# Performance work log

Measured on AMD Instinct MI355X. Metric: run time of the kernel, lower is better.

Reference implementation:

```python
import jax, jax.numpy as jnp
import numpy as np

N_PAPER, N_AUTHOR, E = 100000, 50000, 1000000
D_PAPER, D_AUTHOR, HID, OUT = 256, 128, 256, 349


def setup_inputs() -> dict:
    key = jax.random.key(0)
    ks = jax.random.split(key, 16)
    s = 0.05
    return {
        'x_paper': jax.random.normal(ks[0], (N_PAPER, D_PAPER), jnp.float32),
        'x_author': jax.random.normal(ks[1], (N_AUTHOR, D_AUTHOR), jnp.float32),
        'cites': jax.random.randint(ks[2], (2, E), 0, N_PAPER, jnp.int64 if jax.config.jax_enable_x64 else jnp.int32),
        'writes_src': jax.random.randint(ks[3], (E,), 0, N_AUTHOR),
        'writes_dst': jax.random.randint(ks[4], (E,), 0, N_PAPER),
        'gcn_W1': jax.random.normal(ks[5], (D_PAPER, HID), jnp.float32) * s,
        'gcn_b1': jnp.zeros((HID,), jnp.float32),
        'sage_Wl1': jax.random.normal(ks[6], (D_AUTHOR, HID), jnp.float32) * s,
        'sage_bl1': jnp.zeros((HID,), jnp.float32),
        'sage_Wr1': jax.random.normal(ks[7], (D_PAPER, HID), jnp.float32) * s,
        'gcn_W2': jax.random.normal(ks[8], (HID, HID), jnp.float32) * s,
        'gcn_b2': jnp.zeros((HID,), jnp.float32),
        'sage_Wl2': jax.random.normal(ks[9], (D_AUTHOR, HID), jnp.float32) * s,
        'sage_bl2': jnp.zeros((HID,), jnp.float32),
        'sage_Wr2': jax.random.normal(ks[10], (HID, HID), jnp.float32) * s,
        'lin_W': jax.random.normal(ks[11], (HID, OUT), jnp.float32) * s,
        'lin_b': jnp.zeros((OUT,), jnp.float32),
    }


def _gcn_conv(x, W, b, src, dst, n):
    # GCNConv with add_self_loops=True, symmetric normalization
    loop = jnp.arange(n, dtype=src.dtype)
    si = jnp.concatenate([src, loop])
    di = jnp.concatenate([dst, loop])
    deg = jax.ops.segment_sum(jnp.ones_like(di, x.dtype), di, n)
    dinv = jnp.where(deg > 0, jax.lax.rsqrt(jnp.maximum(deg, 1.0)), 0.0)
    norm = dinv[si] * dinv[di]  # [E+n]
    h = x @ W                   # [n, hid]
    out = jax.ops.segment_sum(h[si] * norm[:, None], di, n)
    return out + b


def _sage_conv(x_src, x_dst, Wl, bl, Wr, src, dst, n_dst):
    # SAGEConv: mean-aggregate neighbors -> lin_l, plus root lin_r (no bias)
    agg = jax.ops.segment_sum(x_src[src], dst, n_dst)
    cnt = jax.ops.segment_sum(jnp.ones_like(dst, x_src.dtype), dst, n_dst)
    mean = agg / jnp.maximum(cnt, 1.0)[:, None]
    return mean @ Wl + bl + x_dst @ Wr


def reference(x_paper, x_author, cites, writes_src, writes_dst,
              gcn_W1, gcn_b1, sage_Wl1, sage_bl1, sage_Wr1,
              gcn_W2, gcn_b2, sage_Wl2, sage_bl2, sage_Wr2,
              lin_W, lin_b):
    n = x_paper.shape[0]
    c_src, c_dst = cites[0], cites[1]
    # layer 1: HeteroConv with aggr='sum' over the two edge-type outputs
    p = jax.nn.relu(
        _gcn_conv(x_paper, gcn_W1, gcn_b1, c_src, c_dst, n)
        + _sage_conv(x_author, x_paper, sage_Wl1, sage_bl1, sage_Wr1, writes_src, writes_dst, n))
    # layer 2 (author features are never updated by these edge types)
    p = jax.nn.relu(
        _gcn_conv(p, gcn_W2, gcn_b2, c_src, c_dst, n)
        + _sage_conv(x_author, p, sage_Wl2, sage_bl2, sage_Wr2, writes_src, writes_dst, n))
    return p @ lin_W + lin_b
```

## Files before the change

kernel.cpp:

```cpp
#include <hip/hip_runtime.h>


#define DP   256
#define DA   128
#define HIDN 256
#define DOUT 349
#define NBKT 782
#define CHUNK 4096

typedef unsigned short u16;
typedef unsigned int u32;
typedef __attribute__((ext_vector_type(8))) short bf16x8;
typedef __attribute__((ext_vector_type(4))) float f32x4;

__device__ __forceinline__ u16 bf16_rn(float x) {
  union { float f; unsigned u; } v; v.f = x;
  unsigned r = v.u + 0x7FFFu + ((v.u >> 16) & 1u);
  return (u16)(r >> 16);
}
__device__ __forceinline__ float bf16f(u16 h) {
  union { float f; unsigned u; } v; v.u = ((unsigned)h) << 16; return v.f;
}
__device__ __forceinline__ unsigned pack2(float a, float b) {
  return (unsigned)bf16_rn(a) | ((unsigned)bf16_rn(b) << 16);
}

__device__ __forceinline__ void gload16(const void* g, void* lds) {
  __builtin_amdgcn_global_load_lds(
      (const __attribute__((address_space(1))) unsigned int*)g,
      (__attribute__((address_space(3))) unsigned int*)lds, 16, 0, 0);
}

#define SCAN_TPB 256
#define SCAN_VPT 8
#define SCAN_TILE 2048

__global__ void scan_local(const int* __restrict__ in, int* __restrict__ out,
                           int* __restrict__ bsum, int n) {
  __shared__ int sdata[SCAN_TPB];
  int t = threadIdx.x;
  int base = blockIdx.x * SCAN_TILE + t * SCAN_VPT;
  int v[SCAN_VPT];
  int sum = 0;
#pragma unroll
  for (int j = 0; j < SCAN_VPT; ++j) {
    int idx = base + j;
    v[j] = (idx < n) ? in[idx] : 0;
    sum += v[j];
  }
  sdata[t] = sum;
  __syncthreads();
  for (int off = 1; off < SCAN_TPB; off <<= 1) {
    int x = (t >= off) ? sdata[t - off] : 0;
    __syncthreads();
    sdata[t] += x;
    __syncthreads();
  }
  int prefix = sdata[t] - sum;
  if (t == SCAN_TPB - 1) bsum[blockIdx.x] = sdata[t];
  int run = prefix;
#pragma unroll
  for (int j = 0; j < SCAN_VPT; ++j) {
    int idx = base + j;
    if (idx < n) out[idx] = run;
    run += v[j];
  }
}

__global__ void scan_spine(int* __restrict__ bsum, int nb) {
  __shared__ int sdata[256];
  int t = threadIdx.x;
  int v = (t < nb) ? bsum[t] : 0;
  sdata[t] = v;
  __syncthreads();
  for (int off = 1; off < 256; off <<= 1) {
    int x = (t >= off) ? sdata[t - off] : 0;
    __syncthreads();
    sdata[t] += x;
    __syncthreads();
  }
  if (t < nb) bsum[t] = sdata[t] - v;
}

__global__ void scan_add(int* __restrict__ out, const int* __restrict__ bsum, int n) {
  int add = bsum[blockIdx.x];
  int base = blockIdx.x * SCAN_TILE + threadIdx.x * SCAN_VPT;
#pragma unroll
  for (int j = 0; j < SCAN_VPT; ++j) {
    int idx = base + j;
    if (idx < n) out[idx] += add;
  }
}

__global__ __launch_bounds__(256) void sort_pass1(
    const int* __restrict__ src, const int* __restrict__ dst,
    uint2* __restrict__ tmp, int* __restrict__ gcount, int* __restrict__ lofs,
    int E, int nch) {
  const int c = blockIdx.x, t = threadIdx.x;
  __shared__ u32 cnt[NBKT];
  __shared__ u32 ofs[NBKT];
  __shared__ u32 sdata[256];
  __shared__ uint2 stage[CHUNK];

  for (int i = t; i < NBKT; i += 256) cnt[i] = 0;
  __syncthreads();
  const int base = c * CHUNK;
#pragma unroll
  for (int j = 0; j < 16; ++j) {
    int i = t + j * 256, idx = base + i;
    if (idx < E) {
      uint2 e; e.x = (u32)src[idx]; e.y = (u32)dst[idx];
      stage[i] = e;
      atomicAdd(&cnt[e.y >> 7], 1u);
    }
  }
  __syncthreads();
  for (int i = t; i < NBKT; i += 256) gcount[(size_t)i * nch + c] = (int)cnt[i];
  u32 ssum = 0;
  const int b0 = t * 4;
#pragma unroll
  for (int j = 0; j < 4; ++j) {
    int i = b0 + j;
    if (i < NBKT) ssum += cnt[i];
  }
  sdata[t] = ssum;
  __syncthreads();
  for (int o = 1; o < 256; o <<= 1) {
    u32 x = (t >= o) ? sdata[t - o] : 0;
    __syncthreads();
    sdata[t] += x;
    __syncthreads();
  }
  u32 run = sdata[t] - ssum;
#pragma unroll
  for (int j = 0; j < 4; ++j) {
    int i = b0 + j;
    if (i < NBKT) { ofs[i] = run; run += cnt[i]; }
  }
  __syncthreads();
  for (int i = t; i < NBKT; i += 256) {
    lofs[(size_t)c * NBKT + i] = (int)ofs[i];
    cnt[i] = ofs[i];
  }
  __syncthreads();
#pragma unroll
  for (int j = 0; j < 16; ++j) {
    int i = t + j * 256, idx = base + i;
    if (idx < E) {
      uint2 e = stage[i];
      u32 p = atomicAdd(&cnt[e.y >> 7], 1u);
      tmp[(size_t)base + p] = e;
    }
  }
}

#define MAXB 2560
__global__ __launch_bounds__(256) void sort_pass2(
    const uint2* __restrict__ tmp, const int* __restrict__ prefix,
    const int* __restrict__ gcount, const int* __restrict__ lofs,
    int* __restrict__ outSorted, int* __restrict__ deg, int* __restrict__ offArr,
    int E, int nch, int n) {
  const int b = blockIdx.x, t = threadIdx.x;
  __shared__ u32 est[MAXB];
  __shared__ u32 outl[MAXB];
  __shared__ u32 cnt[128], ofs[128];
  __shared__ u32 sdata[256];

  const int node0 = b << 7;
  const int ebase = prefix[(size_t)b * nch];
  const int eend = (b == (int)gridDim.x - 1) ? E : prefix[(size_t)(b + 1) * nch];
  const int esize = eend - ebase;

  for (int c = t; c < nch; c += 256) {
    int g = lofs[(size_t)c * NBKT + b];
    int len = gcount[(size_t)b * nch + c];
    int dp = prefix[(size_t)b * nch + c] - ebase;
    for (int k = 0; k < len; ++k) {
      uint2 e = tmp[(size_t)c * CHUNK + g + k];
      est[dp + k] = (e.x << 7) | (e.y & 127u);
    }
  }
  if (t < 128) cnt[t] = 0;
  __syncthreads();
  for (int i = t; i < esize; i += 256) atomicAdd(&cnt[est[i] & 127u], 1u);
  __syncthreads();
  u32 v = (t < 128) ? cnt[t] : 0;
  sdata[t] = v;
  __syncthreads();
  for (int o = 1; o < 256; o <<= 1) {
    u32 x = (t >= o) ? sdata[t - o] : 0;
    __syncthreads();
    sdata[t] += x;
    __syncthreads();
  }
  if (t < 128) ofs[t] = sdata[t] - v;
  __syncthreads();
  const int nNodes = (n - node0) < 128 ? (n - node0) : 128;
  if (t < nNodes) {
    deg[node0 + t] = (int)cnt[t];
    offArr[node0 + t] = ebase + (int)ofs[t];
  }
  __syncthreads();
  if (t < 128) cnt[t] = ofs[t];
  __syncthreads();
  for (int i = t; i < esize; i += 256) {
    u32 e = est[i];
    u32 p = atomicAdd(&cnt[e & 127u], 1u);
    outl[p] = e >> 7;
  }
  __syncthreads();
  for (int i = t; i < esize; i += 256) outSorted[ebase + i] = (int)outl[i];
}

__global__ void conv_bf16(const float* __restrict__ x, u16* __restrict__ o, int n8) {
  int i = blockIdx.x * blockDim.x + threadIdx.x;
  if (i >= n8) return;
  const float4* x4 = (const float4*)x;
  float4 v0 = x4[(size_t)i * 2];
  float4 v1 = x4[(size_t)i * 2 + 1];
  uint4 O;
  O.x = pack2(v0.x, v0.y);
  O.y = pack2(v0.z, v0.w);
  O.z = pack2(v1.x, v1.y);
  O.w = pack2(v1.z, v1.w);
  ((uint4*)o)[i] = O;
}

__global__ void prep_weight(const float* __restrict__ W, int K, int N, int Npad,
                            u16* __restrict__ Bt) {
  int idx = blockIdx.x * blockDim.x + threadIdx.x;
  int tot = Npad * K;
  if (idx >= tot) return;
  int n = idx / K, k = idx - n * K;
  float v = (n < N) ? W[(size_t)k * N + n] : 0.f;
  Bt[idx] = bf16_rn(v);
}

__global__ void pad_bias(const float* __restrict__ a, const float* __restrict__ b,
                         float* __restrict__ o, int n, int npad) {
  int i = blockIdx.x * blockDim.x + threadIdx.x;
  if (i < npad) o[i] = (i < n) ? (a[i] + (b ? b[i] : 0.f)) : 0.f;
}

__global__ void node_prep(const u16* __restrict__ xa16,
                          const int* __restrict__ w_off, const int* __restrict__ w_cnt,
                          const int* __restrict__ w_sorted,
                          const int* __restrict__ deg_c,
                          u16* __restrict__ mean, float* __restrict__ dinv, int n) {
  int wave = (blockIdx.x * blockDim.x + threadIdx.x) >> 6;
  int lane = threadIdx.x & 63;
  if (wave >= n) return;
  int d = wave;
  int start = w_off[d];
  int cnt = w_cnt[d];
  float ax = 0.f, ay = 0.f;
  const unsigned* xa = (const unsigned*)xa16;
  for (int j0 = 0; j0 < cnt; j0 += 64) {
    int nn = cnt - j0; nn = nn < 64 ? nn : 64;
    int sl = (j0 + lane < cnt) ? w_sorted[start + j0 + lane] : 0;
    int jj = 0;
    for (; jj + 4 <= nn; jj += 4) {
      int s0 = __shfl(sl, jj), s1 = __shfl(sl, jj + 1);
      int s2 = __shfl(sl, jj + 2), s3 = __shfl(sl, jj + 3);
      unsigned v0 = xa[(size_t)s0 * 64 + lane];
      unsigned v1 = xa[(size_t)s1 * 64 + lane];
      unsigned v2 = xa[(size_t)s2 * 64 + lane];
      unsigned v3 = xa[(size_t)s3 * 64 + lane];
      ax += bf16f((u16)v0) + bf16f((u16)v1) + bf16f((u16)v2) + bf16f((u16)v3);
      ay += bf16f((u16)(v0 >> 16)) + bf16f((u16)(v1 >> 16)) +
            bf16f((u16)(v2 >> 16)) + bf16f((u16)(v3 >> 16));
    }
    for (; jj < nn; ++jj) {
      int s = __shfl(sl, jj);
      unsigned v = xa[(size_t)s * 64 + lane];
      ax += bf16f((u16)v);
      ay += bf16f((u16)(v >> 16));
    }
  }
  float inv = 1.0f / (float)((cnt > 0) ? cnt : 1);
  ((unsigned*)mean)[(size_t)d * 64 + lane] = pack2(ax * inv, ay * inv);
  if (lane == 0) dinv[d] = rsqrtf((float)(deg_c[d] + 1));
}

__global__ void agg_gcn(const u16* __restrict__ xin, const float* __restrict__ dinv,
                        const int* __restrict__ c_off, const int* __restrict__ c_cnt,
                        const int* __restrict__ c_sorted,
                        u16* __restrict__ xout, int n) {
  int wave = (blockIdx.x * blockDim.x + threadIdx.x) >> 6;
  int lane = threadIdx.x & 63;
  if (wave >= n) return;
  int d = wave;
  int start = c_off[d], cnt = c_cnt[d];
  float a0 = 0.f, a1 = 0.f, a2 = 0.f, a3 = 0.f;
  const uint2* base = (const uint2*)xin;
  for (int j0 = 0; j0 < cnt; j0 += 64) {
    int nn = cnt - j0; nn = nn < 64 ? nn : 64;
    int sl = (j0 + lane < cnt) ? c_sorted[start + j0 + lane] : 0;
    int jj = 0;
    for (; jj + 4 <= nn; jj += 4) {
      int s0 = __shfl(sl, jj), s1 = __shfl(sl, jj + 1);
      int s2 = __shfl(sl, jj + 2), s3 = __shfl(sl, jj + 3);
      float d0 = dinv[s0], d1 = dinv[s1], d2 = dinv[s2], d3 = dinv[s3];
      uint2 v0 = base[(size_t)s0 * 64 + lane];
      uint2 v1 = base[(size_t)s1 * 64 + lane];
      uint2 v2 = base[(size_t)s2 * 64 + lane];
      uint2 v3 = base[(size_t)s3 * 64 + lane];
      a0 = fmaf(bf16f((u16)v0.x), d0, a0); a1 = fmaf(bf16f((u16)(v0.x >> 16)), d0, a1);
      a2 = fmaf(bf16f((u16)v0.y), d0, a2); a3 = fmaf(bf16f((u16)(v0.y >> 16)), d0, a3);
      a0 = fmaf(bf16f((u16)v1.x), d1, a0); a1 = fmaf(bf16f((u16)(v1.x >> 16)), d1, a1);
      a2 = fmaf(bf16f((u16)v1.y), d1, a2); a3 = fmaf(bf16f((u16)(v1.y >> 16)), d1, a3);
      a0 = fmaf(bf16f((u16)v2.x), d2, a0); a1 = fmaf(bf16f((u16)(v2.x >> 16)), d2, a1);
      a2 = fmaf(bf16f((u16)v2.y), d2, a2); a3 = fmaf(bf16f((u16)(v2.y >> 16)), d2, a3);
      a0 = fmaf(bf16f((u16)v3.x), d3, a0); a1 = fmaf(bf16f((u16)(v3.x >> 16)), d3, a1);
      a2 = fmaf(bf16f((u16)v3.y), d3, a2); a3 = fmaf(bf16f((u16)(v3.y >> 16)), d3, a3);
    }
    for (; jj < nn; ++jj) {
      int s = __shfl(sl, jj);
      float ds = dinv[s];
      uint2 v = base[(size_t)s * 64 + lane];
      a0 = fmaf(bf16f((u16)v.x), ds, a0); a1 = fmaf(bf16f((u16)(v.x >> 16)), ds, a1);
      a2 = fmaf(bf16f((u16)v.y), ds, a2); a3 = fmaf(bf16f((u16)(v.y >> 16)), ds, a3);
    }
  }
  float dd = dinv[d];
  {
    uint2 v = base[(size_t)d * 64 + lane];
    a0 = fmaf(bf16f((u16)v.x), dd, a0); a1 = fmaf(bf16f((u16)(v.x >> 16)), dd, a1);
    a2 = fmaf(bf16f((u16)v.y), dd, a2); a3 = fmaf(bf16f((u16)(v.y >> 16)), dd, a3);
  }
  uint2 O;
  O.x = pack2(a0 * dd, a1 * dd);
  O.y = pack2(a2 * dd, a3 * dd);
  ((uint2*)xout)[(size_t)d * 64 + lane] = O;
}

template <int NSEG, bool F32OUT, int NC>
__global__ __launch_bounds__(512, 4) void gemm_bf16(
    const u16* __restrict__ A0, const u16* __restrict__ A1, const u16* __restrict__ A2,
    const u16* __restrict__ B0, const u16* __restrict__ B1, const u16* __restrict__ B2,
    const float* __restrict__ bias,
    u16* __restrict__ Cp, float* __restrict__ Cf,
    int M, int N) {
  __shared__ u16 Ah[2][4096];
  __shared__ u16 Bh[2][8192];

  const int t = threadIdx.x;
  const int wid = t >> 6, lane = t & 63;
  const int wr = wid >> 2, wc = wid & 3;
  const int lrow = lane & 15, kslot = lane >> 4;
  const int jsw = kslot ^ ((lrow >> 1) & 3);

  const int nb = gridDim.x;
  const int q = nb >> 3, r = nb & 7;
  const int xcd = blockIdx.x & 7, pos = blockIdx.x >> 3;
  const int lin = (xcd < r ? xcd * (q + 1) : r * (q + 1) + (xcd - r) * q) + pos;
  const int bx = lin / NC, by = lin - bx * NC;
  const int gm = bx * 128;
  const int gn = by * 256;

  const int s_r = lane >> 2;
  const int s_j = (lane & 3) ^ ((s_r >> 1) & 3);

  f32x4 acc[4][4];
  const f32x4 z4 = {0.f, 0.f, 0.f, 0.f};
#pragma unroll
  for (int m = 0; m < 4; ++m)
#pragma unroll
    for (int n = 0; n < 4; ++n) acc[m][n] = z4;

  const int NT = (NSEG == 3) ? 20 : 8;

  auto STAGE = [&](int tt, int half) {
    const u16* A;
    const u16* B;
    int rs, k0;
    if (NSEG == 3 && tt >= 16)     { A = A2; B = B2; rs = 128; k0 = (tt - 16) * 32; }
    else if (NSEG == 3 && tt >= 8) { A = A1; B = B1; rs = 256; k0 = (tt - 8) * 32; }
    else                           { A = A0; B = B0; rs = 256; k0 = tt * 32; }
    {
      int grow = gm + wid * 16 + s_r;
      grow = grow < M ? grow : M - 1;
      gload16(A + (size_t)grow * rs + (k0 + s_j * 8), &Ah[half][wid * 512]);
    }
#pragma unroll
    for (int c = 0; c < 2; ++c) {
      int chunk = wid * 2 + c;
      int col = gn + chunk * 16 + s_r;
      gload16(B + (size_t)col * rs + (k0 + s_j * 8), &Bh[half][chunk * 512]);
    }
  };

  STAGE(0, 0);
  __syncthreads();

  for (int tt = 0; tt < NT; ++tt) {
    const int half = tt & 1;
    if (tt + 1 < NT) STAGE(tt + 1, half ^ 1);

    bf16x8 ah[4];
    const int ab = (wr * 64 + lrow) * 32 + jsw * 8;
#pragma unroll
    for (int m = 0; m < 4; ++m) ah[m] = *(const bf16x8*)&Ah[half][ab + m * 512];
    const int bb = (wc * 64 + lrow) * 32 + jsw * 8;
#pragma unroll
    for (int n = 0; n < 4; ++n) {
      bf16x8 bn = *(const bf16x8*)&Bh[half][bb + n * 512];
#pragma unroll
      for (int m = 0; m < 4; ++m)
        acc[m][n] = __builtin_amdgcn_mfma_f32_16x16x32_bf16(ah[m], bn, acc[m][n], 0, 0, 0);
    }
    __syncthreads();
  }

  const int col0 = gn + wc * 64 + lrow;
  const int row00 = gm + wr * 64 + kslot * 4;
#pragma unroll
  for (int m = 0; m < 4; ++m) {
#pragma unroll
    for (int i = 0; i < 4; ++i) {
      int row = row00 + m * 16 + i;
      if (row >= M) continue;
#pragma unroll
      for (int n = 0; n < 4; ++n) {
        int col = col0 + n * 16;
        float v = acc[m][n][i] + bias[col];
        if (F32OUT) {
          if (col < N) Cf[(size_t)row * N + col] = v;
        } else {
          Cp[(size_t)row * 256 + col] = bf16_rn(fmaxf(v, 0.f));
        }
      }
    }
  }
}

static inline size_t align_up(size_t x) { return (x + 255) & ~(size_t)255; }

extern "C" void kernel_launch(void* const* d_in, const int* in_sizes, int n_in,
                              void* d_out, int out_size, void* d_ws, size_t ws_size,
                              hipStream_t stream) {
  const float* x_paper  = (const float*)d_in[0];
  const float* x_author = (const float*)d_in[1];
  const int*   cites    = (const int*)d_in[2];
  const int*   w_src    = (const int*)d_in[3];
  const int*   w_dst    = (const int*)d_in[4];
  const float* W1  = (const float*)d_in[5];
  const float* b1  = (const float*)d_in[6];
  const float* Wl1 = (const float*)d_in[7];
  const float* bl1 = (const float*)d_in[8];
  const float* Wr1 = (const float*)d_in[9];
  const float* W2  = (const float*)d_in[10];
  const float* b2  = (const float*)d_in[11];
  const float* Wl2 = (const float*)d_in[12];
  const float* bl2 = (const float*)d_in[13];
  const float* Wr2 = (const float*)d_in[14];
  const float* linW = (const float*)d_in[15];
  const float* linb = (const float*)d_in[16];
  float* out = (float*)d_out;

  const int N = in_sizes[0] / DP;
  const int NA = in_sizes[1] / DA;
  const int E = in_sizes[3];
  const int* c_src = cites;
  const int* c_dst = cites + E;

  const int NCH = (E + CHUNK - 1) / CHUNK;
  const int NB = (N + 127) >> 7;
  const int GC = NB * NCH;

  char* w = (char*)d_ws;
  size_t off = 0;
  auto alloc = [&](size_t bytes) -> void* {
    void* p = w + off;
    off = align_up(off + bytes);
    return p;
  };
  int* deg_c      = (int*)alloc((size_t)N * 4);
  int* cnt_w      = (int*)alloc((size_t)N * 4);
  int* cites_off  = (int*)alloc((size_t)N * 4);
  int* writes_off = (int*)alloc((size_t)N * 4);
  int* c_sorted   = (int*)alloc((size_t)E * 4);
  int* w_sorted   = (int*)alloc((size_t)E * 4);
  uint2* tmpE     = (uint2*)alloc((size_t)NCH * CHUNK * 8);
  int* gcount     = (int*)alloc((size_t)GC * 4);
  int* gprefix    = (int*)alloc((size_t)GC * 4);
  int* lofs       = (int*)alloc((size_t)NCH * NBKT * 4);
  int* bsumA      = (int*)alloc(256 * 4);
  float* dinv     = (float*)alloc((size_t)N * 4);
  u16* xa16       = (u16*)alloc((size_t)NA * DA * 2);
  u16* meanA      = (u16*)alloc((size_t)N * DA * 2);
  u16* xp         = (u16*)alloc((size_t)N * 256 * 2);
  u16* xs         = (u16*)alloc((size_t)N * 256 * 2);
  u16* pb         = (u16*)alloc((size_t)N * 256 * 2);
  const int bsW = 256 * 256, bsL = 256 * 128, bsLin = 512 * 256;
  u16* BtW1  = (u16*)alloc((size_t)bsW * 2);
  u16* BtWr1 = (u16*)alloc((size_t)bsW * 2);
  u16* BtW2  = (u16*)alloc((size_t)bsW * 2);
  u16* BtWr2 = (u16*)alloc((size_t)bsW * 2);
  u16* BtWl1 = (u16*)alloc((size_t)bsL * 2);
  u16* BtWl2 = (u16*)alloc((size_t)bsL * 2);
  u16* BtLin = (u16*)alloc((size_t)bsLin * 2);
  float* biasR1  = (float*)alloc(256 * 4);
  float* biasR2  = (float*)alloc(256 * 4);
  float* biasLin = (float*)alloc(512 * 4);
  (void)ws_size; (void)n_in; (void)out_size;

  const int nsb2 = (GC + SCAN_TILE - 1) / SCAN_TILE;

  sort_pass1<<<NCH, 256, 0, stream>>>(c_src, c_dst, tmpE, gcount, lofs, E, NCH);
  scan_local<<<nsb2, SCAN_TPB, 0, stream>>>(gcount, gprefix, bsumA, GC);
  scan_spine<<<1, 256, 0, stream>>>(bsumA, nsb2);
  scan_add<<<nsb2, SCAN_TPB, 0, stream>>>(gprefix, bsumA, GC);
  sort_pass2<<<NB, 256, 0, stream>>>(tmpE, gprefix, gcount, lofs,
                                     c_sorted, deg_c, cites_off, E, NCH, N);

  conv_bf16<<<(N * 32 + 255) / 256, 256, 0, stream>>>(x_paper, xp, N * 32);
  conv_bf16<<<(NA * 16 + 255) / 256, 256, 0, stream>>>(x_author, xa16, NA * 16);

  sort_pass1<<<NCH, 256, 0, stream>>>(w_src, w_dst, tmpE, gcount, lofs, E, NCH);
  scan_local<<<nsb2, SCAN_TPB, 0, stream>>>(gcount, gprefix, bsumA, GC);
  scan_spine<<<1, 256, 0, stream>>>(bsumA, nsb2);
  scan_add<<<nsb2, SCAN_TPB, 0, stream>>>(gprefix, bsumA, GC);
  sort_pass2<<<NB, 256, 0, stream>>>(tmpE, gprefix, gcount, lofs,
                                     w_sorted, cnt_w, writes_off, E, NCH, N);

  prep_weight<<<(bsW + 255) / 256, 256, 0, stream>>>(W1, 256, 256, 256, BtW1);
  prep_weight<<<(bsW + 255) / 256, 256, 0, stream>>>(Wr1, 256, 256, 256, BtWr1);
  prep_weight<<<(bsW + 255) / 256, 256, 0, stream>>>(W2, 256, 256, 256, BtW2);
  prep_weight<<<(bsW + 255) / 256, 256, 0, stream>>>(Wr2, 256, 256, 256, BtWr2);
  prep_weight<<<(bsL + 255) / 256, 256, 0, stream>>>(Wl1, 128, 256, 256, BtWl1);
  prep_weight<<<(bsL + 255) / 256, 256, 0, stream>>>(Wl2, 128, 256, 256, BtWl2);
  prep_weight<<<(bsLin + 255) / 256, 256, 0, stream>>>(linW, 256, DOUT, 512, BtLin);
  pad_bias<<<1, 256, 0, stream>>>(b1, bl1, biasR1, 256, 256);
  pad_bias<<<1, 256, 0, stream>>>(b2, bl2, biasR2, 256, 256);
  pad_bias<<<2, 256, 0, stream>>>(linb, nullptr, biasLin, DOUT, 512);

  int nbWave = (N * 64 + 255) / 256;
  node_prep<<<nbWave, 256, 0, stream>>>(xa16, writes_off, cnt_w, w_sorted,
                                        deg_c, meanA, dinv, N);

  const int GX = (N + 127) / 128;

  agg_gcn<<<nbWave, 256, 0, stream>>>(xp, dinv, cites_off, deg_c, c_sorted, xs, N);
  gemm_bf16<3, false, 1><<<GX, 512, 0, stream>>>(
      xs, xp, meanA, BtW1, BtWr1, BtWl1, biasR1, pb, nullptr, N, HIDN);
  agg_gcn<<<nbWave, 256, 0, stream>>>(pb, dinv, cites_off, deg_c, c_sorted, xs, N);
  gemm_bf16<3, false, 1><<<GX, 512, 0, stream>>>(
      xs, pb, meanA, BtW2, BtWr2, BtWl2, biasR2, xp, nullptr, N, HIDN);
  gemm_bf16<1, true, 2><<<GX * 2, 512, 0, stream>>>(
      xp, nullptr, nullptr, BtLin, nullptr, nullptr, biasLin, nullptr, out, N, DOUT);
}
```

Before: 542.2 us.

## Batch both edge sorts, fuse first gathers, shrink GEMM tile to 128x128

Both edge-type sorts now run as single launches with doubled grids, and the GCN dinv is computed inside the second sort pass. The author-mean gather and the first GCN aggregation run in one fused launch instead of two. The GEMM tile drops from 128x256 with 512 threads to 128x128 with 256 threads, and the output padding shrinks from 512 to 384 columns. Together these cut launch count, serialization and padded GEMM work, at the cost of more GEMM blocks and lower per-block B reuse.

```diff
diff --git a/kernel.cpp b/kernel.cpp
--- a/kernel.cpp
+++ b/kernel.cpp
@@ -93,10 +93,15 @@
 }
 
 __global__ __launch_bounds__(256) void sort_pass1(
-    const int* __restrict__ src, const int* __restrict__ dst,
+    const int* __restrict__ c_src, const int* __restrict__ c_dst,
+    const int* __restrict__ w_srcP, const int* __restrict__ w_dstP,
     uint2* __restrict__ tmp, int* __restrict__ gcount, int* __restrict__ lofs,
     int E, int nch) {
-  const int c = blockIdx.x, t = threadIdx.x;
+  const int cg = blockIdx.x, t = threadIdx.x;
+  const int et = cg >= nch;
+  const int c = cg - et * nch;
+  const int* src = et ? w_srcP : c_src;
+  const int* dst = et ? w_dstP : c_dst;
   __shared__ u32 cnt[NBKT];
   __shared__ u32 ofs[NBKT];
   __shared__ u32 sdata[256];
@@ -115,7 +120,8 @@
     }
   }
   __syncthreads();
-  for (int i = t; i < NBKT; i += 256) gcount[(size_t)i * nch + c] = (int)cnt[i];
+  for (int i = t; i < NBKT; i += 256)
+    gcount[((size_t)et * NBKT + i) * nch + c] = (int)cnt[i];
   u32 ssum = 0;
   const int b0 = t * 4;
 #pragma unroll
@@ -139,17 +145,18 @@
   }
   __syncthreads();
   for (int i = t; i < NBKT; i += 256) {
-    lofs[(size_t)c * NBKT + i] = (int)ofs[i];
+    lofs[((size_t)et * nch + c) * NBKT + i] = (int)ofs[i];
     cnt[i] = ofs[i];
   }
   __syncthreads();
+  uint2* tout = tmp + (size_t)et * nch * CHUNK + base;
 #pragma unroll
   for (int j = 0; j < 16; ++j) {
     int i = t + j * 256, idx = base + i;
     if (idx < E) {
       uint2 e = stage[i];
       u32 p = atomicAdd(&cnt[e.y >> 7], 1u);
-      tmp[(size_t)base + p] = e;
+      tout[p] = e;
     }
   }
 }
@@ -158,25 +165,35 @@
 __global__ __launch_bounds__(256) void sort_pass2(
     const uint2* __restrict__ tmp, const int* __restrict__ prefix,
     const int* __restrict__ gcount, const int* __restrict__ lofs,
-    int* __restrict__ outSorted, int* __restrict__ deg, int* __restrict__ offArr,
-    int E, int nch, int n) {
-  const int b = blockIdx.x, t = threadIdx.x;
+    int* __restrict__ cSorted, int* __restrict__ cDeg, int* __restrict__ cOff,
+    int* __restrict__ wSorted, int* __restrict__ wDeg, int* __restrict__ wOff,
+    float* __restrict__ dinv,
+    int E, int nch, int n, int nbk) {
+  const int bg = blockIdx.x, t = threadIdx.x;
+  const int et = bg >= nbk;
+  const int b = bg - et * nbk;
+  int* outSorted = et ? wSorted : cSorted;
+  int* deg = et ? wDeg : cDeg;
+  int* offArr = et ? wOff : cOff;
   __shared__ u32 est[MAXB];
   __shared__ u32 outl[MAXB];
   __shared__ u32 cnt[128], ofs[128];
   __shared__ u32 sdata[256];
 
   const int node0 = b << 7;
-  const int ebase = prefix[(size_t)b * nch];
-  const int eend = (b == (int)gridDim.x - 1) ? E : prefix[(size_t)(b + 1) * nch];
-  const int esize = eend - ebase;
-
+  const size_t bgl = (size_t)et * NBKT + b;
+  const int ebaseG = prefix[bgl * nch];
+  const int eendG = (bg == 2 * nbk - 1) ? 2 * E : prefix[(bgl + 1) * nch];
+  const int ebase = ebaseG - et * E;
+  const int esize = (eendG - et * E) - ebase;
+
+  const uint2* tsrc = tmp + (size_t)et * nch * CHUNK;
   for (int c = t; c < nch; c += 256) {
-    int g = lofs[(size_t)c * NBKT + b];
-    int len = gcount[(size_t)b * nch + c];
-    int dp = prefix[(size_t)b * nch + c] - ebase;
+    int g = lofs[((size_t)et * nch + c) * NBKT + b];
+    int len = gcount[bgl * nch + c];
+    int dp = prefix[bgl * nch + c] - ebaseG;
     for (int k = 0; k < len; ++k) {
-      uint2 e = tmp[(size_t)c * CHUNK + g + k];
+      uint2 e = tsrc[(size_t)c * CHUNK + g + k];
       est[dp + k] = (e.x << 7) | (e.y & 127u);
     }
   }
@@ -199,6 +216,7 @@
   if (t < nNodes) {
     deg[node0 + t] = (int)cnt[t];
     offArr[node0 + t] = ebase + (int)ofs[t];
+    if (et == 0) dinv[node0 + t] = rsqrtf((float)(cnt[t] + 1));
   }
   __syncthreads();
   if (t < 128) cnt[t] = ofs[t];
@@ -242,44 +260,93 @@
   if (i < npad) o[i] = (i < n) ? (a[i] + (b ? b[i] : 0.f)) : 0.f;
 }
 
-__global__ void node_prep(const u16* __restrict__ xa16,
-                          const int* __restrict__ w_off, const int* __restrict__ w_cnt,
-                          const int* __restrict__ w_sorted,
-                          const int* __restrict__ deg_c,
-                          u16* __restrict__ mean, float* __restrict__ dinv, int n) {
-  int wave = (blockIdx.x * blockDim.x + threadIdx.x) >> 6;
-  int lane = threadIdx.x & 63;
-  if (wave >= n) return;
-  int d = wave;
-  int start = w_off[d];
-  int cnt = w_cnt[d];
-  float ax = 0.f, ay = 0.f;
-  const unsigned* xa = (const unsigned*)xa16;
-  for (int j0 = 0; j0 < cnt; j0 += 64) {
-    int nn = cnt - j0; nn = nn < 64 ? nn : 64;
-    int sl = (j0 + lane < cnt) ? w_sorted[start + j0 + lane] : 0;
-    int jj = 0;
-    for (; jj + 4 <= nn; jj += 4) {
-      int s0 = __shfl(sl, jj), s1 = __shfl(sl, jj + 1);
-      int s2 = __shfl(sl, jj + 2), s3 = __shfl(sl, jj + 3);
-      unsigned v0 = xa[(size_t)s0 * 64 + lane];
-      unsigned v1 = xa[(size_t)s1 * 64 + lane];
-      unsigned v2 = xa[(size_t)s2 * 64 + lane];
-      unsigned v3 = xa[(size_t)s3 * 64 + lane];
-      ax += bf16f((u16)v0) + bf16f((u16)v1) + bf16f((u16)v2) + bf16f((u16)v3);
-      ay += bf16f((u16)(v0 >> 16)) + bf16f((u16)(v1 >> 16)) +
-            bf16f((u16)(v2 >> 16)) + bf16f((u16)(v3 >> 16));
-    }
-    for (; jj < nn; ++jj) {
-      int s = __shfl(sl, jj);
-      unsigned v = xa[(size_t)s * 64 + lane];
-      ax += bf16f((u16)v);
-      ay += bf16f((u16)(v >> 16));
-    }
-  }
-  float inv = 1.0f / (float)((cnt > 0) ? cnt : 1);
-  ((unsigned*)mean)[(size_t)d * 64 + lane] = pack2(ax * inv, ay * inv);
-  if (lane == 0) dinv[d] = rsqrtf((float)(deg_c[d] + 1));
+__global__ void gather_fused(
+    const u16* __restrict__ xin, const float* __restrict__ dinv,
+    const int* __restrict__ c_off, const int* __restrict__ c_cnt,
+    const int* __restrict__ c_sorted, u16* __restrict__ xout,
+    const u16* __restrict__ xa16, const int* __restrict__ w_off,
+    const int* __restrict__ w_cnt, const int* __restrict__ w_sorted,
+    u16* __restrict__ mean, int n, int nbw) {
+  const int lane = threadIdx.x & 63;
+  if (blockIdx.x < nbw) {
+    int wave = ((blockIdx.x * blockDim.x) >> 6) + (threadIdx.x >> 6);
+    if (wave >= n) return;
+    int d = wave;
+    int start = c_off[d], cnt = c_cnt[d];
+    float a0 = 0.f, a1 = 0.f, a2 = 0.f, a3 = 0.f;
+    const uint2* base = (const uint2*)xin;
+    for (int j0 = 0; j0 < cnt; j0 += 64) {
+      int nn = cnt - j0; nn = nn < 64 ? nn : 64;
+      int sl = (j0 + lane < cnt) ? c_sorted[start + j0 + lane] : 0;
+      int jj = 0;
+      for (; jj + 4 <= nn; jj += 4) {
+        int s0 = __shfl(sl, jj), s1 = __shfl(sl, jj + 1);
+        int s2 = __shfl(sl, jj + 2), s3 = __shfl(sl, jj + 3);
+        float d0 = dinv[s0], d1 = dinv[s1], d2 = dinv[s2], d3 = dinv[s3];
+        uint2 v0 = base[(size_t)s0 * 64 + lane];
+        uint2 v1 = base[(size_t)s1 * 64 + lane];
+        uint2 v2 = base[(size_t)s2 * 64 + lane];
+        uint2 v3 = base[(size_t)s3 * 64 + lane];
+        a0 = fmaf(bf16f((u16)v0.x), d0, a0); a1 = fmaf(bf16f((u16)(v0.x >> 16)), d0, a1);
+        a2 = fmaf(bf16f((u16)v0.y), d0, a2); a3 = fmaf(bf16f((u16)(v0.y >> 16)), d0, a3);
+        a0 = fmaf(bf16f((u16)v1.x), d1, a0); a1 = fmaf(bf16f((u16)(v1.x >> 16)), d1, a1);
+        a2 = fmaf(bf16f((u16)v1.y), d1, a2); a3 = fmaf(bf16f((u16)(v1.y >> 16)), d1, a3);
+        a0 = fmaf(bf16f((u16)v2.x), d2, a0); a1 = fmaf(bf16f((u16)(v2.x >> 16)), d2, a1);
+        a2 = fmaf(bf16f((u16)v2.y), d2, a2); a3 = fmaf(bf16f((u16)(v2.y >> 16)), d2, a3);
+        a0 = fmaf(bf16f((u16)v3.x), d3, a0); a1 = fmaf(bf16f((u16)(v3.x >> 16)), d3, a1);
+        a2 = fmaf(bf16f((u16)v3.y), d3, a2); a3 = fmaf(bf16f((u16)(v3.y >> 16)), d3, a3);
+      }
+      for (; jj < nn; ++jj) {
+        int s = __shfl(sl, jj);
+        float ds = dinv[s];
+        uint2 v = base[(size_t)s * 64 + lane];
+        a0 = fmaf(bf16f((u16)v.x), ds, a0); a1 = fmaf(bf16f((u16)(v.x >> 16)), ds, a1);
+        a2 = fmaf(bf16f((u16)v.y), ds, a2); a3 = fmaf(bf16f((u16)(v.y >> 16)), ds, a3);
+      }
+    }
+    float dd = dinv[d];
+    {
+      uint2 v = base[(size_t)d * 64 + lane];
+      a0 = fmaf(bf16f((u16)v.x), dd, a0); a1 = fmaf(bf16f((u16)(v.x >> 16)), dd, a1);
+      a2 = fmaf(bf16f((u16)v.y), dd, a2); a3 = fmaf(bf16f((u16)(v.y >> 16)), dd, a3);
+    }
+    uint2 O;
+    O.x = pack2(a0 * dd, a1 * dd);
+    O.y = pack2(a2 * dd, a3 * dd);
+    ((uint2*)xout)[(size_t)d * 64 + lane] = O;
+  } else {
+    int wave = (((blockIdx.x - nbw) * blockDim.x) >> 6) + (threadIdx.x >> 6);
+    if (wave >= n) return;
+    int d = wave;
+    int start = w_off[d];
+    int cnt = w_cnt[d];
+    float ax = 0.f, ay = 0.f;
+    const unsigned* xa = (const unsigned*)xa16;
+    for (int j0 = 0; j0 < cnt; j0 += 64) {
+      int nn = cnt - j0; nn = nn < 64 ? nn : 64;
+      int sl = (j0 + lane < cnt) ? w_sorted[start + j0 + lane] : 0;
+      int jj = 0;
+      for (; jj + 4 <= nn; jj += 4) {
+        int s0 = __shfl(sl, jj), s1 = __shfl(sl, jj + 1);
+        int s2 = __shfl(sl, jj + 2), s3 = __shfl(sl, jj + 3);
+        unsigned v0 = xa[(size_t)s0 * 64 + lane];
+        unsigned v1 = xa[(size_t)s1 * 64 + lane];
+        unsigned v2 = xa[(size_t)s2 * 64 + lane];
+        unsigned v3 = xa[(size_t)s3 * 64 + lane];
+        ax += bf16f((u16)v0) + bf16f((u16)v1) + bf16f((u16)v2) + bf16f((u16)v3);
+        ay += bf16f((u16)(v0 >> 16)) + bf16f((u16)(v1 >> 16)) +
+              bf16f((u16)(v2 >> 16)) + bf16f((u16)(v3 >> 16));
+      }
+      for (; jj < nn; ++jj) {
+        int s = __shfl(sl, jj);
+        unsigned v = xa[(size_t)s * 64 + lane];
+        ax += bf16f((u16)v);
+        ay += bf16f((u16)(v >> 16));
+      }
+    }
+    float inv = 1.0f / (float)((cnt > 0) ? cnt : 1);
+    ((unsigned*)mean)[(size_t)d * 64 + lane] = pack2(ax * inv, ay * inv);
+  }
 }
 
 __global__ void agg_gcn(const u16* __restrict__ xin, const float* __restrict__ dinv,
@@ -335,18 +402,18 @@
 }
 
 template <int NSEG, bool F32OUT, int NC>
-__global__ __launch_bounds__(512, 4) void gemm_bf16(
+__global__ __launch_bounds__(256, 4) void gemm_bf16(
     const u16* __restrict__ A0, const u16* __restrict__ A1, const u16* __restrict__ A2,
     const u16* __restrict__ B0, const u16* __restrict__ B1, const u16* __restrict__ B2,
     const float* __restrict__ bias,
     u16* __restrict__ Cp, float* __restrict__ Cf,
     int M, int N) {
   __shared__ u16 Ah[2][4096];
-  __shared__ u16 Bh[2][8192];
+  __shared__ u16 Bh[2][4096];
 
   const int t = threadIdx.x;
   const int wid = t >> 6, lane = t & 63;
-  const int wr = wid >> 2, wc = wid & 3;
+  const int wr = wid >> 1, wc = wid & 1;
   const int lrow = lane & 15, kslot = lane >> 4;
   const int jsw = kslot ^ ((lrow >> 1) & 3);
 
@@ -356,7 +423,7 @@
   const int lin = (xcd < r ? xcd * (q + 1) : r * (q + 1) + (xcd - r) * q) + pos;
   const int bx = lin / NC, by = lin - bx * NC;
   const int gm = bx * 128;
-  const int gn = by * 256;
+  const int gn = by * 128;
 
   const int s_r = lane >> 2;
   const int s_j = (lane & 3) ^ ((s_r >> 1) & 3);
@@ -377,16 +444,14 @@
     if (NSEG == 3 && tt >= 16)     { A = A2; B = B2; rs = 128; k0 = (tt - 16) * 32; }
     else if (NSEG == 3 && tt >= 8) { A = A1; B = B1; rs = 256; k0 = (tt - 8) * 32; }
     else                           { A = A0; B = B0; rs = 256; k0 = tt * 32; }
-    {
-      int grow = gm + wid * 16 + s_r;
+    const int c = wid * 2;
+#pragma unroll
+    for (int cc = 0; cc < 2; ++cc) {
+      int grow = gm + (c + cc) * 16 + s_r;
       grow = grow < M ? grow : M - 1;
-      gload16(A + (size_t)grow * rs + (k0 + s_j * 8), &Ah[half][wid * 512]);
-    }
-#pragma unroll
-    for (int c = 0; c < 2; ++c) {
-      int chunk = wid * 2 + c;
-      int col = gn + chunk * 16 + s_r;
-      gload16(B + (size_t)col * rs + (k0 + s_j * 8), &Bh[half][chunk * 512]);
+      gload16(A + (size_t)grow * rs + (k0 + s_j * 8), &Ah[half][(c + cc) * 512]);
+      int col = gn + (c + cc) * 16 + s_r;
+      gload16(B + (size_t)col * rs + (k0 + s_j * 8), &Bh[half][(c + cc) * 512]);
     }
   };
 
@@ -466,7 +531,7 @@
 
   const int NCH = (E + CHUNK - 1) / CHUNK;
   const int NB = (N + 127) >> 7;
-  const int GC = NB * NCH;
+  const int GC2 = 2 * NB * NCH;
 
   char* w = (char*)d_ws;
   size_t off = 0;
@@ -481,10 +546,10 @@
   int* writes_off = (int*)alloc((size_t)N * 4);
   int* c_sorted   = (int*)alloc((size_t)E * 4);
   int* w_sorted   = (int*)alloc((size_t)E * 4);
-  uint2* tmpE     = (uint2*)alloc((size_t)NCH * CHUNK * 8);
-  int* gcount     = (int*)alloc((size_t)GC * 4);
-  int* gprefix    = (int*)alloc((size_t)GC * 4);
-  int* lofs       = (int*)alloc((size_t)NCH * NBKT * 4);
+  uint2* tmpE     = (uint2*)alloc((size_t)2 * NCH * CHUNK * 8);
+  int* gcount     = (int*)alloc((size_t)GC2 * 4);
+  int* gprefix    = (int*)alloc((size_t)GC2 * 4);
+  int* lofs       = (int*)alloc((size_t)2 * NCH * NBKT * 4);
   int* bsumA      = (int*)alloc(256 * 4);
   float* dinv     = (float*)alloc((size_t)N * 4);
   u16* xa16       = (u16*)alloc((size_t)NA * DA * 2);
@@ -492,7 +557,7 @@
   u16* xp         = (u16*)alloc((size_t)N * 256 * 2);
   u16* xs         = (u16*)alloc((size_t)N * 256 * 2);
   u16* pb         = (u16*)alloc((size_t)N * 256 * 2);
-  const int bsW = 256 * 256, bsL = 256 * 128, bsLin = 512 * 256;
+  const int bsW = 256 * 256, bsL = 256 * 128, bsLin = 384 * 256;
   u16* BtW1  = (u16*)alloc((size_t)bsW * 2);
   u16* BtWr1 = (u16*)alloc((size_t)bsW * 2);
   u16* BtW2  = (u16*)alloc((size_t)bsW * 2);
@@ -502,27 +567,23 @@
   u16* BtLin = (u16*)alloc((size_t)bsLin * 2);
   float* biasR1  = (float*)alloc(256 * 4);
   float* biasR2  = (float*)alloc(256 * 4);
-  float* biasLin = (float*)alloc(512 * 4);
+  float* biasLin = (float*)alloc(384 * 4);
   (void)ws_size; (void)n_in; (void)out_size;
 
-  const int nsb2 = (GC + SCAN_TILE - 1) / SCAN_TILE;
-
-  sort_pass1<<<NCH, 256, 0, stream>>>(c_src, c_dst, tmpE, gcount, lofs, E, NCH);
-  scan_local<<<nsb2, SCAN_TPB, 0, stream>>>(gcount, gprefix, bsumA, GC);
+  const int nsb2 = (GC2 + SCAN_TILE - 1) / SCAN_TILE;
+
+  sort_pass1<<<2 * NCH, 256, 0, stream>>>(c_src, c_dst, w_src, w_dst,
+                                          tmpE, gcount, lofs, E, NCH);
+  scan_local<<<nsb2, SCAN_TPB, 0, stream>>>(gcount, gprefix, bsumA, GC2);
   scan_spine<<<1, 256, 0, stream>>>(bsumA, nsb2);
-  scan_add<<<nsb2, SCAN_TPB, 0, stream>>>(gprefix, bsumA, GC);
-  sort_pass2<<<NB, 256, 0, stream>>>(tmpE, gprefix, gcount, lofs,
-                                     c_sorted, deg_c, cites_off, E, NCH, N);
+  scan_add<<<nsb2, SCAN_TPB, 0, stream>>>(gprefix, bsumA, GC2);
+  sort_pass2<<<2 * NB, 256, 0, stream>>>(tmpE, gprefix, gcount, lofs,
+                                         c_sorted, deg_c, cites_off,
+                                         w_sorted, cnt_w, writes_off,
+                                         dinv, E, NCH, N, NB);
 
   conv_bf16<<<(N * 32 + 255) / 256, 256, 0, stream>>>(x_paper, xp, N * 32);
   conv_bf16<<<(NA * 16 + 255) / 256, 256, 0, stream>>>(x_author, xa16, NA * 16);
-
-  sort_pass1<<<NCH, 256, 0, stream>>>(w_src, w_dst, tmpE, gcount, lofs, E, NCH);
-  scan_local<<<nsb2, SCAN_TPB, 0, stream>>>(gcount, gprefix, bsumA, GC);
-  scan_spine<<<1, 256, 0, stream>>>(bsumA, nsb2);
-  scan_add<<<nsb2, SCAN_TPB, 0, stream>>>(gprefix, bsumA, GC);
-  sort_pass2<<<NB, 256, 0, stream>>>(tmpE, gprefix, gcount, lofs,
-                                     w_sorted, cnt_w, writes_off, E, NCH, N);
 
   prep_weight<<<(bsW + 255) / 256, 256, 0, stream>>>(W1, 256, 256, 256, BtW1);
   prep_weight<<<(bsW + 255) / 256, 256, 0, stream>>>(Wr1, 256, 256, 256, BtWr1);
@@ -530,23 +591,22 @@
   prep_weight<<<(bsW + 255) / 256, 256, 0, stream>>>(Wr2, 256, 256, 256, BtWr2);
   prep_weight<<<(bsL + 255) / 256, 256, 0, stream>>>(Wl1, 128, 256, 256, BtWl1);
   prep_weight<<<(bsL + 255) / 256, 256, 0, stream>>>(Wl2, 128, 256, 256, BtWl2);
-  prep_weight<<<(bsLin + 255) / 256, 256, 0, stream>>>(linW, 256, DOUT, 512, BtLin);
+  prep_weight<<<(bsLin + 255) / 256, 256, 0, stream>>>(linW, 256, DOUT, 384, BtLin);
   pad_bias<<<1, 256, 0, stream>>>(b1, bl1, biasR1, 256, 256);
   pad_bias<<<1, 256, 0, stream>>>(b2, bl2, biasR2, 256, 256);
-  pad_bias<<<2, 256, 0, stream>>>(linb, nullptr, biasLin, DOUT, 512);
-
-  int nbWave = (N * 64 + 255) / 256;
-  node_prep<<<nbWave, 256, 0, stream>>>(xa16, writes_off, cnt_w, w_sorted,
-                                        deg_c, meanA, dinv, N);
-
+  pad_bias<<<2, 256, 0, stream>>>(linb, nullptr, biasLin, DOUT, 384);
+
+  const int nbWave = (N * 64 + 255) / 256;
   const int GX = (N + 127) / 128;
 
-  agg_gcn<<<nbWave, 256, 0, stream>>>(xp, dinv, cites_off, deg_c, c_sorted, xs, N);
-  gemm_bf16<3, false, 1><<<GX, 512, 0, stream>>>(
+  gather_fused<<<2 * nbWave, 256, 0, stream>>>(
+      xp, dinv, cites_off, deg_c, c_sorted, xs,
+      xa16, writes_off, cnt_w, w_sorted, meanA, N, nbWave);
+  gemm_bf16<3, false, 2><<<GX * 2, 256, 0, stream>>>(
       xs, xp, meanA, BtW1, BtWr1, BtWl1, biasR1, pb, nullptr, N, HIDN);
   agg_gcn<<<nbWave, 256, 0, stream>>>(pb, dinv, cites_off, deg_c, c_sorted, xs, N);
-  gemm_bf16<3, false, 1><<<GX, 512, 0, stream>>>(
+  gemm_bf16<3, false, 2><<<GX * 2, 256, 0, stream>>>(
       xs, pb, meanA, BtW2, BtWr2, BtWl2, biasR2, xp, nullptr, N, HIDN);
-  gemm_bf16<1, true, 2><<<GX * 2, 512, 0, stream>>>(
+  gemm_bf16<1, true, 3><<<GX * 3, 256, 0, stream>>>(
       xp, nullptr, nullptr, BtLin, nullptr, nullptr, biasLin, nullptr, out, N, DOUT);
 }
```

New measurement: 493.2 us. 1.1x faster.
